# Kernel optimization log

Measured on AMD Instinct MI355X. Metric: run time of the kernel, lower is better.

The kernel has to match this reference:

```python
import jax, jax.numpy as jnp
import numpy as np

N_NODES = 50000
N_EDGES = 800000
IN_DIM = 128
HID = 64
HEADS = 4
OUT_DIM = 128
NEG_SLOPE = 0.2


def setup_inputs() -> dict:
    key = jax.random.key(0)
    ks = jax.random.split(key, 11)
    x = jax.random.normal(ks[0], (N_NODES, IN_DIM), dtype=jnp.float32)
    edge_index = jax.random.randint(ks[1], (2, N_EDGES), 0, N_NODES, dtype=jnp.int64)
    s1 = 1.0 / np.sqrt(IN_DIM)
    s2 = 1.0 / np.sqrt(HEADS * HID)
    W1 = jax.random.normal(ks[2], (IN_DIM, HEADS * HID), dtype=jnp.float32) * s1
    a_src1 = jax.random.normal(ks[3], (HEADS, HID), dtype=jnp.float32) * s2
    a_dst1 = jax.random.normal(ks[4], (HEADS, HID), dtype=jnp.float32) * s2
    b1 = jnp.zeros((HEADS * HID,), dtype=jnp.float32)
    W2 = jax.random.normal(ks[5], (HEADS * HID, OUT_DIM), dtype=jnp.float32) * s2
    a_src2 = jax.random.normal(ks[6], (1, OUT_DIM), dtype=jnp.float32) * 0.1
    a_dst2 = jax.random.normal(ks[7], (1, OUT_DIM), dtype=jnp.float32) * 0.1
    b2 = jnp.zeros((OUT_DIM,), dtype=jnp.float32)
    return {"x": x, "edge_index": edge_index, "W1": W1, "a_src1": a_src1,
            "a_dst1": a_dst1, "b1": b1, "W2": W2, "a_src2": a_src2,
            "a_dst2": a_dst2, "b2": b2}


def _gat_conv(x, src, dst, W, a_src, a_dst, bias, heads, out_per_head, concat):
    n = x.shape[0]
    # linear projection per head: [N, H, F]
    h = (x @ W).reshape(n, heads, out_per_head)
    # per-node attention terms: [N, H]
    alpha_src = jnp.einsum('nhf,hf->nh', h, a_src)
    alpha_dst = jnp.einsum('nhf,hf->nh', h, a_dst)
    # edge logits with LeakyReLU: [E, H]
    e = jax.nn.leaky_relu(alpha_src[src] + alpha_dst[dst], NEG_SLOPE)
    # softmax over incoming edges of each destination node
    m = jax.ops.segment_max(e, dst, num_segments=n)  # [N, H]
    m = jnp.where(jnp.isfinite(m), m, 0.0)
    e = jnp.exp(e - m[dst])
    denom = jax.ops.segment_sum(e, dst, num_segments=n)  # [N, H]
    alpha = e / (denom[dst] + 1e-16)  # [E, H]
    # weighted scatter-aggregate of source messages
    out = jax.ops.segment_sum(h[src] * alpha[:, :, None], dst, num_segments=n)  # [N, H, F]
    if concat:
        out = out.reshape(n, heads * out_per_head)
    else:
        out = out.mean(axis=1)
    return out + bias


def reference(x, edge_index, W1, a_src1, a_dst1, b1, W2, a_src2, a_dst2, b2):
    n = x.shape[0]
    # PyG GATConv adds self-loops by default
    loops = jnp.arange(n, dtype=edge_index.dtype)
    src = jnp.concatenate([edge_index[0], loops])
    dst = jnp.concatenate([edge_index[1], loops])
    # dropout layers are identity in inference
    h = _gat_conv(x, src, dst, W1, a_src1, a_dst1, b1, HEADS, HID, True)
    h = jax.nn.elu(h)
    out = _gat_conv(h, src, dst, W2, a_src2, a_dst2, b2, 1, OUT_DIM, True)
    # F.normalize(p=2, dim=1)
    norm = jnp.linalg.norm(out, axis=1, keepdims=True)
    return out / jnp.maximum(norm, 1e-12)
```

## Files before the change

### kernel.cpp

```cpp
#include <hip/hip_runtime.h>
#include <hip/hip_fp16.h>
#include <math.h>

#define N_NODES 50000
#define N_EDGES 800000
#define ET (N_EDGES + N_NODES)
#define IN_DIM 128
#define HID 64
#define HEADS 4
#define C1 (HEADS * HID)
#define OUT_DIM 128
#define NEG_SLOPE 0.2f
#define MTILES 3125
#define SCAN_B 1024
#define NSCB 49
#define SCB 3328
#define FUSED_GRID 4160

typedef _Float16 h8 __attribute__((ext_vector_type(8)));
typedef float f4 __attribute__((ext_vector_type(4)));
typedef unsigned short u16;

__device__ __forceinline__ float leaky(float v) { return fmaxf(v, NEG_SLOPE * v); }
__device__ __forceinline__ float elu(float v) { return v > 0.0f ? v : expm1f(v); }

__device__ __forceinline__ void fma_mix8(float* acc, h8 v, float w) {
    union { h8 h; int i[4]; } u; u.h = v;
#pragma unroll
    for (int k = 0; k < 4; ++k) {
        asm("v_fma_mix_f32 %0, %1, %2, %0 op_sel:[0,0,0] op_sel_hi:[1,0,0]"
            : "+v"(acc[2 * k]) : "v"(u.i[k]), "v"(w));
        asm("v_fma_mix_f32 %0, %1, %2, %0 op_sel:[1,0,0] op_sel_hi:[1,0,0]"
            : "+v"(acc[2 * k + 1]) : "v"(u.i[k]), "v"(w));
    }
}

__global__ void prep_kernel(const float* __restrict__ W1, const float* __restrict__ W2,
                            const int* __restrict__ dst, __half* __restrict__ w1t,
                            __half* __restrict__ w2t, int* __restrict__ cnt) {
    const int tid = blockIdx.x * blockDim.x + threadIdx.x;
    const int np = gridDim.x * blockDim.x;
    for (int i = tid; i < IN_DIM * C1; i += np) {
        int k1 = i >> 8, n1 = i & 255;
        w1t[n1 * IN_DIM + k1] = __float2half(W1[i]);
        int k2 = i >> 7, n2 = i & 127;
        w2t[n2 * C1 + k2] = __float2half(W2[i]);
    }
    for (int i = tid; i < ET; i += np) {
        int d = (i < N_EDGES) ? dst[i] : i - N_EDGES;
        atomicAdd(&cnt[d], 1);
    }
}

__global__ void scan_local(const int* __restrict__ cnt, int* __restrict__ lscan,
                           int* __restrict__ bsum) {
    __shared__ int wsum[16];
    const int t = threadIdx.x, lane = t & 63, wv = t >> 6;
    int idx = blockIdx.x * SCAN_B + t;
    int v = (idx < N_NODES) ? cnt[idx] : 0;
    int sc = v;
#pragma unroll
    for (int o = 1; o < 64; o <<= 1) {
        int u = __shfl_up(sc, o);
        if (lane >= o) sc += u;
    }
    if (lane == 63) wsum[wv] = sc;
    __syncthreads();
    if (t == 0) {
        int run = 0;
#pragma unroll
        for (int w = 0; w < 16; ++w) { int s = wsum[w]; wsum[w] = run; run += s; }
        bsum[blockIdx.x] = run;
    }
    __syncthreads();
    if (idx < N_NODES) lscan[idx] = sc + wsum[wv];
}

__global__ void scan_bsum(int* __restrict__ bsum) {
    const int t = threadIdx.x;
    int v = (t < NSCB) ? bsum[t] : 0;
    int sc = v;
#pragma unroll
    for (int o = 1; o < 64; o <<= 1) {
        int u = __shfl_up(sc, o);
        if (t >= o) sc += u;
    }
    if (t < NSCB) bsum[t] = sc - v;
}

__global__ void scan_final(const int* __restrict__ cnt, const int* __restrict__ lscan,
                           const int* __restrict__ bsum, int* __restrict__ rp,
                           int* __restrict__ cursor) {
    int idx = blockIdx.x * SCAN_B + threadIdx.x;
    if (idx == 0) rp[0] = 0;
    if (idx >= N_NODES) return;
    int inc = lscan[idx] + bsum[idx >> 10];
    rp[idx + 1] = inc;
    cursor[idx] = inc - cnt[idx];
}

__global__ __launch_bounds__(256) void gemm1_scatter(
        const float* __restrict__ x, const __half* __restrict__ w1t,
        const float* __restrict__ aws, const float* __restrict__ awd,
        __half* __restrict__ hpm, float* __restrict__ as1m, float* __restrict__ ad1m,
        const int* __restrict__ src, const int* __restrict__ dst,
        int* __restrict__ cursor, u16* __restrict__ cs16) {
    const int q5 = blockIdx.x / 5, r5 = blockIdx.x % 5;
    if (r5 != 0) {
        int si = q5 * 4 + (r5 - 1);
        int i = si * 256 + threadIdx.x;
        if (i < ET) {
            int s, d;
            if (i < N_EDGES) { s = src[i]; d = dst[i]; } else { s = d = i - N_EDGES; }
            int pos = atomicAdd(&cursor[d], 1);
            cs16[pos] = (u16)s;
        }
        return;
    }
    const int tile = q5 * 4 + (threadIdx.x >> 6);
    if (tile >= MTILES) return;
    const int lane = threadIdx.x & 63;
    const int m0 = tile * 16, lm = lane & 15, lq = lane >> 4;
    h8 afrag[4];
    const float4* xrow = (const float4*)(x + (size_t)(m0 + lm) * IN_DIM + lq * 8);
#pragma unroll
    for (int kt = 0; kt < 4; ++kt) {
        float4 a = xrow[kt * 8];
        float4 b = xrow[kt * 8 + 1];
        union { h8 v; __half2 p[4]; } u;
        u.p[0] = __floats2half2_rn(a.x, a.y);
        u.p[1] = __floats2half2_rn(a.z, a.w);
        u.p[2] = __floats2half2_rn(b.x, b.y);
        u.p[3] = __floats2half2_rn(b.z, b.w);
        afrag[kt] = u.v;
    }
    f4 acc[16];
#pragma unroll
    for (int nt = 0; nt < 16; ++nt) acc[nt] = (f4){0.f, 0.f, 0.f, 0.f};
#pragma unroll
    for (int nt = 0; nt < 16; ++nt) {
        const h8* brow = (const h8*)(w1t + (size_t)(nt * 16 + lm) * IN_DIM + lq * 8);
#pragma unroll
        for (int kt = 0; kt < 4; ++kt)
            acc[nt] = __builtin_amdgcn_mfma_f32_16x16x32_f16(afrag[kt], brow[kt * 4],
                                                             acc[nt], 0, 0, 0);
    }
    float sS[4][4] = {{0.f}}, sD[4][4] = {{0.f}};
#pragma unroll
    for (int nt = 0; nt < 16; ++nt) {
        int col = nt * 16 + lm;
        float wa = aws[col], wd = awd[col];
        int hd = nt >> 2;
        int pr = nt >> 3;
        int cip = col & 127;
#pragma unroll
        for (int r = 0; r < 4; ++r) {
            float v = acc[nt][r];
            hpm[((size_t)pr * N_NODES + (m0 + lq * 4 + r)) * 128 + cip] = __float2half(v);
            sS[hd][r] += v * wa;
            sD[hd][r] += v * wd;
        }
    }
#pragma unroll
    for (int o = 1; o < 16; o <<= 1) {
#pragma unroll
        for (int hd = 0; hd < 4; ++hd)
#pragma unroll
            for (int r = 0; r < 4; ++r) {
                sS[hd][r] += __shfl_xor(sS[hd][r], o);
                sD[hd][r] += __shfl_xor(sD[hd][r], o);
            }
    }
    if (lm == 0) {
        float2* asp = (float2*)as1m;
        float2* adp = (float2*)ad1m;
#pragma unroll
        for (int r = 0; r < 4; ++r) {
            int row = m0 + lq * 4 + r;
            asp[row]           = make_float2(sS[0][r], sS[1][r]);
            asp[N_NODES + row] = make_float2(sS[2][r], sS[3][r]);
            adp[row]           = make_float2(sD[0][r], sD[1][r]);
            adp[N_NODES + row] = make_float2(sD[2][r], sD[3][r]);
        }
    }
}

__global__ __launch_bounds__(256) void gemm2_mfma(
        const __half* __restrict__ ah, const __half* __restrict__ w2t,
        const float* __restrict__ aws, const float* __restrict__ awd,
        __half* __restrict__ h, float* __restrict__ as2, float* __restrict__ ad2) {
    const int tile = blockIdx.x * 4 + (threadIdx.x >> 6);
    if (tile >= MTILES) return;
    const int lane = threadIdx.x & 63;
    const int m0 = tile * 16, lm = lane & 15, lq = lane >> 4;
    h8 afrag[8];
    const h8* arow = (const h8*)(ah + (size_t)(m0 + lm) * C1 + lq * 8);
#pragma unroll
    for (int kt = 0; kt < 8; ++kt) afrag[kt] = arow[kt * 4];
    f4 acc[8];
#pragma unroll
    for (int nt = 0; nt < 8; ++nt) acc[nt] = (f4){0.f, 0.f, 0.f, 0.f};
#pragma unroll
    for (int nt = 0; nt < 8; ++nt) {
        const h8* brow = (const h8*)(w2t + (size_t)(nt * 16 + lm) * C1 + lq * 8);
#pragma unroll
        for (int kt = 0; kt < 8; ++kt)
            acc[nt] = __builtin_amdgcn_mfma_f32_16x16x32_f16(afrag[kt], brow[kt * 4],
                                                             acc[nt], 0, 0, 0);
    }
    float sS[4] = {0.f, 0.f, 0.f, 0.f}, sD[4] = {0.f, 0.f, 0.f, 0.f};
#pragma unroll
    for (int nt = 0; nt < 8; ++nt) {
        int col = nt * 16 + lm;
        float wa = aws[col], wd = awd[col];
#pragma unroll
        for (int r = 0; r < 4; ++r) {
            float v = acc[nt][r];
            h[(size_t)(m0 + lq * 4 + r) * OUT_DIM + col] = __float2half(v);
            sS[r] += v * wa;
            sD[r] += v * wd;
        }
    }
#pragma unroll
    for (int o = 1; o < 16; o <<= 1) {
#pragma unroll
        for (int r = 0; r < 4; ++r) {
            sS[r] += __shfl_xor(sS[r], o);
            sD[r] += __shfl_xor(sD[r], o);
        }
    }
    if (lm == 0) {
#pragma unroll
        for (int r = 0; r < 4; ++r) {
            int row = m0 + lq * 4 + r;
            as2[row] = sS[r];
            ad2[row] = sD[r];
        }
    }
}

__global__ __launch_bounds__(256) void aggregate1_fused(
        const int* __restrict__ rp, const u16* __restrict__ cs16,
        const __half* __restrict__ hpm, const float* __restrict__ as1m,
        const float* __restrict__ ad1m, const float* __restrict__ b1,
        __half* __restrict__ out1h) {
    __shared__ int4 stg[8][32];
    const int pair = blockIdx.x & 1, g = blockIdx.x >> 1;
    const int hw = threadIdx.x >> 5, li = threadIdx.x & 31;
    const int d = g * 8 + hw;
    const int e0 = rp[d], deg = rp[d + 1] - e0;
    const float2* asb = (const float2*)as1m + (size_t)pair * N_NODES;
    const float2 adv = ((const float2*)ad1m)[(size_t)pair * N_NODES + d];
    const char* hb = (const char*)hpm + (size_t)pair * N_NODES * 256;
    const int es = li >> 4, fl = li & 15;
    const int hip = fl >> 3;
    const int lbyte = fl * 16;
    float acc[8] = {0.f, 0.f, 0.f, 0.f, 0.f, 0.f, 0.f, 0.f};
    float ds0 = 0.f, ds1 = 0.f;
    for (int c0 = 0; c0 < deg; c0 += 32) {
        const int clen = min(32, deg - c0);
        int idx = c0 + li;
        bool valid = idx < deg;
        int s = valid ? (int)cs16[e0 + idx] : 0;
        float2 av = asb[s];
        float x0 = valid ? __expf(leaky(av.x + adv.x)) : 0.f;
        float x1 = valid ? __expf(leaky(av.y + adv.y)) : 0.f;
        stg[hw][li] = make_int4(s << 8, __float_as_int(x0), __float_as_int(x1), 0);
        ds0 += x0; ds1 += x1;
        __builtin_amdgcn_wave_barrier();
        int j = 0;
        for (; j + 16 <= clen; j += 16) {
            int4 p0 = stg[hw][j + es];
            int4 p1 = stg[hw][j + 2 + es];
            int4 p2 = stg[hw][j + 4 + es];
            int4 p3 = stg[hw][j + 6 + es];
            int4 p4 = stg[hw][j + 8 + es];
            int4 p5 = stg[hw][j + 10 + es];
            int4 p6 = stg[hw][j + 12 + es];
            int4 p7 = stg[hw][j + 14 + es];
            h8 v0 = *(const h8*)(hb + p0.x + lbyte);
            h8 v1 = *(const h8*)(hb + p1.x + lbyte);
            h8 v2 = *(const h8*)(hb + p2.x + lbyte);
            h8 v3 = *(const h8*)(hb + p3.x + lbyte);
            h8 v4 = *(const h8*)(hb + p4.x + lbyte);
            h8 v5 = *(const h8*)(hb + p5.x + lbyte);
            h8 v6 = *(const h8*)(hb + p6.x + lbyte);
            h8 v7 = *(const h8*)(hb + p7.x + lbyte);
            fma_mix8(acc, v0, __int_as_float(hip ? p0.z : p0.y));
            fma_mix8(acc, v1, __int_as_float(hip ? p1.z : p1.y));
            fma_mix8(acc, v2, __int_as_float(hip ? p2.z : p2.y));
            fma_mix8(acc, v3, __int_as_float(hip ? p3.z : p3.y));
            fma_mix8(acc, v4, __int_as_float(hip ? p4.z : p4.y));
            fma_mix8(acc, v5, __int_as_float(hip ? p5.z : p5.y));
            fma_mix8(acc, v6, __int_as_float(hip ? p6.z : p6.y));
            fma_mix8(acc, v7, __int_as_float(hip ? p7.z : p7.y));
        }
        for (; j + 8 <= clen; j += 8) {
            int4 p0 = stg[hw][j + es];
            int4 p1 = stg[hw][j + 2 + es];
            int4 p2 = stg[hw][j + 4 + es];
            int4 p3 = stg[hw][j + 6 + es];
            h8 v0 = *(const h8*)(hb + p0.x + lbyte);
            h8 v1 = *(const h8*)(hb + p1.x + lbyte);
            h8 v2 = *(const h8*)(hb + p2.x + lbyte);
            h8 v3 = *(const h8*)(hb + p3.x + lbyte);
            fma_mix8(acc, v0, __int_as_float(hip ? p0.z : p0.y));
            fma_mix8(acc, v1, __int_as_float(hip ? p1.z : p1.y));
            fma_mix8(acc, v2, __int_as_float(hip ? p2.z : p2.y));
            fma_mix8(acc, v3, __int_as_float(hip ? p3.z : p3.y));
        }
        for (; j < clen; j += 2) {
            int4 p0 = stg[hw][j + es];
            h8 v0 = *(const h8*)(hb + p0.x + lbyte);
            fma_mix8(acc, v0, __int_as_float(hip ? p0.z : p0.y));
        }
        __builtin_amdgcn_wave_barrier();
    }
#pragma unroll
    for (int f = 0; f < 8; ++f) acc[f] += __shfl_xor(acc[f], 16);
#pragma unroll
    for (int o = 16; o > 0; o >>= 1) {
        ds0 += __shfl_xor(ds0, o);
        ds1 += __shfl_xor(ds1, o);
    }
    if (es == 0) {
        float den = hip ? ds1 : ds0;
        float inv = 1.0f / (den + 1e-16f);
        float4 bA = ((const float4*)b1)[pair * 32 + fl * 2];
        float4 bB = ((const float4*)b1)[pair * 32 + fl * 2 + 1];
        h8 o;
        o[0] = (_Float16)elu(acc[0] * inv + bA.x);
        o[1] = (_Float16)elu(acc[1] * inv + bA.y);
        o[2] = (_Float16)elu(acc[2] * inv + bA.z);
        o[3] = (_Float16)elu(acc[3] * inv + bA.w);
        o[4] = (_Float16)elu(acc[4] * inv + bB.x);
        o[5] = (_Float16)elu(acc[5] * inv + bB.y);
        o[6] = (_Float16)elu(acc[6] * inv + bB.z);
        o[7] = (_Float16)elu(acc[7] * inv + bB.w);
        *(h8*)((char*)out1h + (size_t)d * 512 + pair * 256 + lbyte) = o;
    }
}

__global__ __launch_bounds__(256) void aggregate2_fused(
        const int* __restrict__ rp, const u16* __restrict__ cs16,
        const __half* __restrict__ h2h, const float* __restrict__ as2,
        const float* __restrict__ ad2, const float* __restrict__ b2,
        float* __restrict__ out) {
    __shared__ int2 stg[8][32];
    const int hw = threadIdx.x >> 5, li = threadIdx.x & 31;
    const int d = blockIdx.x * 8 + hw;
    const int e0 = rp[d], deg = rp[d + 1] - e0;
    const float adv = ad2[d];
    const int q = li >> 4, lo = li & 15;
    const int lbyte = lo * 16;
    const char* hbase = (const char*)h2h;
    float acc[8] = {0.f, 0.f, 0.f, 0.f, 0.f, 0.f, 0.f, 0.f};
    float dsum = 0.f;
    for (int c0 = 0; c0 < deg; c0 += 32) {
        const int clen = min(32, deg - c0);
        int idx = c0 + li;
        bool valid = idx < deg;
        int s = valid ? (int)cs16[e0 + idx] : 0;
        float xv = valid ? __expf(leaky(as2[s] + adv)) : 0.f;
        stg[hw][li] = make_int2(s << 8, __float_as_int(xv));
        dsum += xv;
        __builtin_amdgcn_wave_barrier();
        int j = 0;
        for (; j + 16 <= clen; j += 16) {
            int2 p0 = stg[hw][j + q];
            int2 p1 = stg[hw][j + 2 + q];
            int2 p2 = stg[hw][j + 4 + q];
            int2 p3 = stg[hw][j + 6 + q];
            int2 p4 = stg[hw][j + 8 + q];
            int2 p5 = stg[hw][j + 10 + q];
            int2 p6 = stg[hw][j + 12 + q];
            int2 p7 = stg[hw][j + 14 + q];
            h8 v0 = *(const h8*)(hbase + p0.x + lbyte);
            h8 v1 = *(const h8*)(hbase + p1.x + lbyte);
            h8 v2 = *(const h8*)(hbase + p2.x + lbyte);
            h8 v3 = *(const h8*)(hbase + p3.x + lbyte);
            h8 v4 = *(const h8*)(hbase + p4.x + lbyte);
            h8 v5 = *(const h8*)(hbase + p5.x + lbyte);
            h8 v6 = *(const h8*)(hbase + p6.x + lbyte);
            h8 v7 = *(const h8*)(hbase + p7.x + lbyte);
            fma_mix8(acc, v0, __int_as_float(p0.y));
            fma_mix8(acc, v1, __int_as_float(p1.y));
            fma_mix8(acc, v2, __int_as_float(p2.y));
            fma_mix8(acc, v3, __int_as_float(p3.y));
            fma_mix8(acc, v4, __int_as_float(p4.y));
            fma_mix8(acc, v5, __int_as_float(p5.y));
            fma_mix8(acc, v6, __int_as_float(p6.y));
            fma_mix8(acc, v7, __int_as_float(p7.y));
        }
        for (; j + 8 <= clen; j += 8) {
            int2 p0 = stg[hw][j + q];
            int2 p1 = stg[hw][j + 2 + q];
            int2 p2 = stg[hw][j + 4 + q];
            int2 p3 = stg[hw][j + 6 + q];
            h8 v0 = *(const h8*)(hbase + p0.x + lbyte);
            h8 v1 = *(const h8*)(hbase + p1.x + lbyte);
            h8 v2 = *(const h8*)(hbase + p2.x + lbyte);
            h8 v3 = *(const h8*)(hbase + p3.x + lbyte);
            fma_mix8(acc, v0, __int_as_float(p0.y));
            fma_mix8(acc, v1, __int_as_float(p1.y));
            fma_mix8(acc, v2, __int_as_float(p2.y));
            fma_mix8(acc, v3, __int_as_float(p3.y));
        }
        for (; j < clen; j += 2) {
            int2 p0 = stg[hw][j + q];
            h8 v0 = *(const h8*)(hbase + p0.x + lbyte);
            fma_mix8(acc, v0, __int_as_float(p0.y));
        }
        __builtin_amdgcn_wave_barrier();
    }
#pragma unroll
    for (int f = 0; f < 8; ++f) acc[f] += __shfl_xor(acc[f], 16);
#pragma unroll
    for (int o = 16; o > 0; o >>= 1) dsum += __shfl_xor(dsum, o);
    if (q == 0) {
        float inv = 1.0f / (dsum + 1e-16f);
        float4 bA = ((const float4*)b2)[lo * 2];
        float4 bB = ((const float4*)b2)[lo * 2 + 1];
        float v0 = acc[0] * inv + bA.x, v1 = acc[1] * inv + bA.y;
        float v2 = acc[2] * inv + bA.z, v3 = acc[3] * inv + bA.w;
        float v4 = acc[4] * inv + bB.x, v5 = acc[5] * inv + bB.y;
        float v6 = acc[6] * inv + bB.z, v7 = acc[7] * inv + bB.w;
        float ss = v0 * v0 + v1 * v1 + v2 * v2 + v3 * v3 +
                   v4 * v4 + v5 * v5 + v6 * v6 + v7 * v7;
#pragma unroll
        for (int o = 1; o < 16; o <<= 1) ss += __shfl_xor(ss, o);
        float sc = 1.0f / fmaxf(sqrtf(ss), 1e-12f);
        float4* orow = (float4*)((char*)out + (size_t)d * 512 + lo * 32);
        orow[0] = make_float4(v0 * sc, v1 * sc, v2 * sc, v3 * sc);
        orow[1] = make_float4(v4 * sc, v5 * sc, v6 * sc, v7 * sc);
    }
}

extern "C" void kernel_launch(void* const* d_in, const int* in_sizes, int n_in,
                              void* d_out, int out_size, void* d_ws, size_t ws_size,
                              hipStream_t stream) {
    const float* x     = (const float*)d_in[0];
    const int*   edge  = (const int*)d_in[1];
    const int*   src   = edge;
    const int*   dst   = edge + N_EDGES;
    const float* W1    = (const float*)d_in[2];
    const float* aw_s1 = (const float*)d_in[3];
    const float* aw_d1 = (const float*)d_in[4];
    const float* b1    = (const float*)d_in[5];
    const float* W2    = (const float*)d_in[6];
    const float* aw_s2 = (const float*)d_in[7];
    const float* aw_d2 = (const float*)d_in[8];
    const float* b2    = (const float*)d_in[9];
    float* out = (float*)d_out;

    char* ws = (char*)d_ws;
    size_t off = 0;
    auto alloc = [&](size_t bytes) {
        void* p = ws + off;
        off += (bytes + 255) & ~(size_t)255;
        return p;
    };
    u16*    cs16   = (u16*)alloc((size_t)ET * 2);
    int*    rp     = (int*)alloc((size_t)(N_NODES + 1) * 4);
    int*    cursor = (int*)alloc((size_t)N_NODES * 4);
    int*    cnt    = (int*)alloc((size_t)N_NODES * 4);
    int*    lscan  = (int*)alloc((size_t)NSCB * SCAN_B * 4);
    int*    bsum   = (int*)alloc((size_t)NSCB * 4);
    float*  as1    = (float*)alloc((size_t)N_NODES * HEADS * 4);
    float*  ad1    = (float*)alloc((size_t)N_NODES * HEADS * 4);
    float*  as2    = (float*)alloc((size_t)N_NODES * 4);
    float*  ad2    = (float*)alloc((size_t)N_NODES * 4);
    __half* w1t    = (__half*)alloc((size_t)IN_DIM * C1 * 2);
    __half* w2t    = (__half*)alloc((size_t)C1 * OUT_DIM * 2);
    __half* hpm    = (__half*)alloc((size_t)N_NODES * C1 * 2);
    __half* out1h  = (__half*)alloc((size_t)N_NODES * C1 * 2);
    __half* h2h    = hpm;
    (void)off;

    hipMemsetAsync(cnt, 0, (size_t)N_NODES * 4, stream);

    prep_kernel<<<1024, 256, 0, stream>>>(W1, W2, dst, w1t, w2t, cnt);
    scan_local<<<NSCB, SCAN_B, 0, stream>>>(cnt, lscan, bsum);
    scan_bsum<<<1, 64, 0, stream>>>(bsum);
    scan_final<<<NSCB, SCAN_B, 0, stream>>>(cnt, lscan, bsum, rp, cursor);

    gemm1_scatter<<<FUSED_GRID, 256, 0, stream>>>(x, w1t, aw_s1, aw_d1, hpm, as1, ad1,
                                                  src, dst, cursor, cs16);

    aggregate1_fused<<<(N_NODES / 8) * 2, 256, 0, stream>>>(rp, cs16, hpm, as1, ad1, b1, out1h);

    gemm2_mfma<<<(MTILES + 3) / 4, 256, 0, stream>>>(out1h, w2t, aw_s2, aw_d2, h2h, as2, ad2);
    aggregate2_fused<<<N_NODES / 8, 256, 0, stream>>>(rp, cs16, h2h, as2, ad2, b2, out);
}
```

Before: 332.1 us.

## Build CSR with rank-from-count atomics and separate atomic-free scatter

The counting pass now records each edge's return value from its atomicAdd as a per-edge rank. A new scatter kernel then places sources at rp[dst]+rank with no atomics, and self-loops go in the last slot of each row. The scatter is split out of the fused gemm1 kernel, which becomes a standalone MFMA GEMM. This removes a second pass of contended atomics on cursor, at the cost of an extra rank buffer and one more kernel launch. Edge order within each row now follows the order the counting atomics happen to resolve in, so it is not deterministic.

```diff
diff --git a/kernel.cpp b/kernel.cpp
--- a/kernel.cpp
+++ b/kernel.cpp
@@ -14,8 +14,6 @@
 #define MTILES 3125
 #define SCAN_B 1024
 #define NSCB 49
-#define SCB 3328
-#define FUSED_GRID 4160
 
 typedef _Float16 h8 __attribute__((ext_vector_type(8)));
 typedef float f4 __attribute__((ext_vector_type(4)));
@@ -37,7 +35,8 @@
 
 __global__ void prep_kernel(const float* __restrict__ W1, const float* __restrict__ W2,
                             const int* __restrict__ dst, __half* __restrict__ w1t,
-                            __half* __restrict__ w2t, int* __restrict__ cnt) {
+                            __half* __restrict__ w2t, int* __restrict__ cnt,
+                            u16* __restrict__ rank16) {
     const int tid = blockIdx.x * blockDim.x + threadIdx.x;
     const int np = gridDim.x * blockDim.x;
     for (int i = tid; i < IN_DIM * C1; i += np) {
@@ -46,9 +45,9 @@
         int k2 = i >> 7, n2 = i & 127;
         w2t[n2 * C1 + k2] = __float2half(W2[i]);
     }
-    for (int i = tid; i < ET; i += np) {
-        int d = (i < N_EDGES) ? dst[i] : i - N_EDGES;
-        atomicAdd(&cnt[d], 1);
+    for (int i = tid; i < N_EDGES; i += np) {
+        int d = dst[i];
+        rank16[i] = (u16)atomicAdd(&cnt[d], 1);
     }
 }
 
@@ -57,7 +56,7 @@
     __shared__ int wsum[16];
     const int t = threadIdx.x, lane = t & 63, wv = t >> 6;
     int idx = blockIdx.x * SCAN_B + t;
-    int v = (idx < N_NODES) ? cnt[idx] : 0;
+    int v = (idx < N_NODES) ? cnt[idx] + 1 : 0;
     int sc = v;
 #pragma unroll
     for (int o = 1; o < 64; o <<= 1) {
@@ -88,36 +87,33 @@
     if (t < NSCB) bsum[t] = sc - v;
 }
 
-__global__ void scan_final(const int* __restrict__ cnt, const int* __restrict__ lscan,
-                           const int* __restrict__ bsum, int* __restrict__ rp,
-                           int* __restrict__ cursor) {
+__global__ void scan_final(const int* __restrict__ lscan, const int* __restrict__ bsum,
+                           int* __restrict__ rp) {
     int idx = blockIdx.x * SCAN_B + threadIdx.x;
     if (idx == 0) rp[0] = 0;
     if (idx >= N_NODES) return;
-    int inc = lscan[idx] + bsum[idx >> 10];
-    rp[idx + 1] = inc;
-    cursor[idx] = inc - cnt[idx];
-}
-
-__global__ __launch_bounds__(256) void gemm1_scatter(
+    rp[idx + 1] = lscan[idx] + bsum[idx >> 10];
+}
+
+__global__ void scatter_plain(const int* __restrict__ src, const int* __restrict__ dst,
+                              const u16* __restrict__ rank16, const int* __restrict__ rp,
+                              u16* __restrict__ cs16) {
+    int i = blockIdx.x * blockDim.x + threadIdx.x;
+    if (i >= ET) return;
+    if (i < N_EDGES) {
+        int d = dst[i];
+        cs16[rp[d] + (int)rank16[i]] = (u16)src[i];
+    } else {
+        int d = i - N_EDGES;
+        cs16[rp[d + 1] - 1] = (u16)d;
+    }
+}
+
+__global__ __launch_bounds__(256) void gemm1_mfma(
         const float* __restrict__ x, const __half* __restrict__ w1t,
         const float* __restrict__ aws, const float* __restrict__ awd,
-        __half* __restrict__ hpm, float* __restrict__ as1m, float* __restrict__ ad1m,
-        const int* __restrict__ src, const int* __restrict__ dst,
-        int* __restrict__ cursor, u16* __restrict__ cs16) {
-    const int q5 = blockIdx.x / 5, r5 = blockIdx.x % 5;
-    if (r5 != 0) {
-        int si = q5 * 4 + (r5 - 1);
-        int i = si * 256 + threadIdx.x;
-        if (i < ET) {
-            int s, d;
-            if (i < N_EDGES) { s = src[i]; d = dst[i]; } else { s = d = i - N_EDGES; }
-            int pos = atomicAdd(&cursor[d], 1);
-            cs16[pos] = (u16)s;
-        }
-        return;
-    }
-    const int tile = q5 * 4 + (threadIdx.x >> 6);
+        __half* __restrict__ hpm, float* __restrict__ as1m, float* __restrict__ ad1m) {
+    const int tile = blockIdx.x * 4 + (threadIdx.x >> 6);
     if (tile >= MTILES) return;
     const int lane = threadIdx.x & 63;
     const int m0 = tile * 16, lm = lane & 15, lq = lane >> 4;
@@ -461,8 +457,8 @@
         return p;
     };
     u16*    cs16   = (u16*)alloc((size_t)ET * 2);
+    u16*    rank16 = (u16*)alloc((size_t)N_EDGES * 2);
     int*    rp     = (int*)alloc((size_t)(N_NODES + 1) * 4);
-    int*    cursor = (int*)alloc((size_t)N_NODES * 4);
     int*    cnt    = (int*)alloc((size_t)N_NODES * 4);
     int*    lscan  = (int*)alloc((size_t)NSCB * SCAN_B * 4);
     int*    bsum   = (int*)alloc((size_t)NSCB * 4);
@@ -479,14 +475,15 @@
 
     hipMemsetAsync(cnt, 0, (size_t)N_NODES * 4, stream);
 
-    prep_kernel<<<1024, 256, 0, stream>>>(W1, W2, dst, w1t, w2t, cnt);
+    const int egrid = (ET + 255) / 256;
+
+    prep_kernel<<<1024, 256, 0, stream>>>(W1, W2, dst, w1t, w2t, cnt, rank16);
     scan_local<<<NSCB, SCAN_B, 0, stream>>>(cnt, lscan, bsum);
     scan_bsum<<<1, 64, 0, stream>>>(bsum);
-    scan_final<<<NSCB, SCAN_B, 0, stream>>>(cnt, lscan, bsum, rp, cursor);
-
-    gemm1_scatter<<<FUSED_GRID, 256, 0, stream>>>(x, w1t, aw_s1, aw_d1, hpm, as1, ad1,
-                                                  src, dst, cursor, cs16);
-
+    scan_final<<<NSCB, SCAN_B, 0, stream>>>(lscan, bsum, rp);
+    scatter_plain<<<egrid, 256, 0, stream>>>(src, dst, rank16, rp, cs16);
+
+    gemm1_mfma<<<(MTILES + 3) / 4, 256, 0, stream>>>(x, w1t, aw_s1, aw_d1, hpm, as1, ad1);
     aggregate1_fused<<<(N_NODES / 8) * 2, 256, 0, stream>>>(rp, cs16, hpm, as1, ad1, b1, out1h);
 
     gemm2_mfma<<<(MTILES + 3) / 4, 256, 0, stream>>>(out1h, w2t, aw_s2, aw_d2, h2h, as2, ad2);
```

New measurement: 310.2 us. 6.6% less time.
